# Kernel optimization log

Hardware: AMD Instinct MI355X
Metric: run time of the kernel (lower is better)

## Reference

```python
import jax, jax.numpy as jnp
import numpy as np

N_TREES, N_LEAVES, PATH_LEN, N_NODES, D, B = 10, 16, 5, 31, 256, 4096


def _local_paths():
    # root-to-leaf paths of a full binary tree, depth 4: 31 nodes, 16 leaves, path len 5
    return np.array([[0, 1 + l // 8, 3 + l // 4, 7 + l // 2, 15 + l]
                     for l in range(N_LEAVES)], np.int32)


def setup_inputs() -> dict:
    key = jax.random.key(0)
    k1, k2, k3, k4, k5, k6 = jax.random.split(key, 6)
    # one activated leaf per tree -> multi-hot cross_features (B, N_TREES*N_LEAVES)
    leaf = jax.random.randint(k1, (B, N_TREES), 0, N_LEAVES)
    cross = jnp.zeros((B, N_TREES, N_LEAVES), jnp.float32)
    cross = cross.at[jnp.arange(B)[:, None], jnp.arange(N_TREES)[None, :], leaf].set(1.0)
    cross_features = cross.reshape(B, N_TREES * N_LEAVES)
    # learned params: node embedding table + single-layer LSTM (torch init scale 1/sqrt(D))
    emb = jax.random.normal(k2, (N_TREES * N_NODES, D), jnp.float32) * 0.02
    s = 1.0 / np.sqrt(D)
    W_ih = jax.random.uniform(k3, (4 * D, D), jnp.float32, -s, s)
    W_hh = jax.random.uniform(k4, (4 * D, D), jnp.float32, -s, s)
    b_ih = jax.random.uniform(k5, (4 * D,), jnp.float32, -s, s)
    b_hh = jax.random.uniform(k6, (4 * D,), jnp.float32, -s, s)
    return {"cross_features": cross_features, "emb": emb, "W_ih": W_ih,
            "W_hh": W_hh, "b_ih": b_ih, "b_hh": b_hh}


def reference(cross_features, emb, W_ih, W_hh, b_ih, b_hh):
    # global path node ids per (tree, leaf): [T, L, P]
    gpaths = jnp.asarray(_local_paths())[None, :, :] + \
        (jnp.arange(N_TREES, dtype=jnp.int32) * N_NODES)[:, None, None]
    # activated leaf per tree (exactly one hot per 16-leaf block)
    leaf = jnp.argmax(cross_features.reshape(B, N_TREES, N_LEAVES), axis=-1)  # [B, T]
    node_ids = gpaths[jnp.arange(N_TREES)[None, :], leaf]                     # [B, T, P]
    x = emb[node_ids].reshape(B * N_TREES, PATH_LEN, D)                       # packed paths
    # precompute input projections for all steps: [N, P, 4D]
    xg = jnp.einsum('npd,gd->npg', x, W_ih) + (b_ih + b_hh)

    def step(carry, xt):
        h, c = carry
        g = xt + h @ W_hh.T
        i, f, gg, o = jnp.split(g, 4, axis=-1)  # torch gate order: i, f, g, o
        c = jax.nn.sigmoid(f) * c + jax.nn.sigmoid(i) * jnp.tanh(gg)
        h = jax.nn.sigmoid(o) * jnp.tanh(c)
        return (h, c), None

    n = B * N_TREES
    h0 = jnp.zeros((n, D), x.dtype)
    (h, _), _ = jax.lax.scan(step, (h0, h0), jnp.swapaxes(xg, 0, 1))
    return h.reshape(B, N_TREES, D)
```

## Files before the change

kernel.cpp:

```cpp
#include <hip/hip_runtime.h>

#define NT 10
#define NL 16
#define NN 31
#define DD 256
#define G4 1024
#define NNODES (NT*NN)
#define NPATH (NT*NL)
#define NB 4096
#define NROWS (NB*NT)

__device__ unsigned g_pg[3][16][32];

__device__ __forceinline__ float sigf(float x)   { return 1.0f / (1.0f + __expf(-x)); }
__device__ __forceinline__ float tanh_f(float x) { return 2.0f / (1.0f + __expf(-2.0f*x)) - 1.0f; }

__device__ __forceinline__ void co_store(float* p, float v) {
    union { float f; unsigned u; } c; c.f = v;
    __hip_atomic_store((unsigned*)p, c.u, __ATOMIC_RELAXED, __HIP_MEMORY_SCOPE_AGENT);
}

__global__ __launch_bounds__(256) void k_nodeproj(
    const float* __restrict__ emb, const float* __restrict__ Wih,
    const float* __restrict__ bih, const float* __restrict__ bhh,
    float* __restrict__ xg)
{
    __shared__ float smem[20 * 260 + 20 * 4 * 64];
    float4* es4 = (float4*)smem;
    float*  ps  = smem + 20 * 260;

    const int tid = threadIdx.x;
    const int nt  = blockIdx.x & 15;
    const int mt  = blockIdx.x >> 4;
    const int kq  = tid >> 6;
    const int w   = tid & 63;

    const float4* W4 = (const float4*)Wih + (size_t)(nt * 64 + w) * 64 + kq * 16;
    float4 wr[16];
    #pragma unroll
    for (int j = 0; j < 16; ++j) wr[j] = W4[j];

    const float4* emb4 = (const float4*)emb;
    #pragma unroll
    for (int r = 0; r < 5; ++r) {
        int idx = tid + 256 * r;
        int m = idx >> 6, q = idx & 63;
        int n = mt * 20 + m;
        es4[m * 65 + q] = (n < NNODES) ? emb4[(size_t)n * 64 + q]
                                       : make_float4(0.f, 0.f, 0.f, 0.f);
    }
    __syncthreads();

    float acc[20];
    #pragma unroll
    for (int m = 0; m < 20; ++m) acc[m] = 0.f;
    #pragma unroll
    for (int j = 0; j < 16; ++j) {
        float4 wv = wr[j];
        #pragma unroll
        for (int m = 0; m < 20; ++m) {
            float4 h = es4[m * 65 + kq * 16 + j];
            acc[m] = fmaf(wv.x, h.x, fmaf(wv.y, h.y,
                     fmaf(wv.z, h.z, fmaf(wv.w, h.w, acc[m]))));
        }
    }
    #pragma unroll
    for (int m = 0; m < 20; ++m) ps[(m * 4 + kq) * 64 + w] = acc[m];
    __syncthreads();

    const int nl   = tid & 63;
    const int msub = tid >> 6;
    const int j    = nt * 64 + nl;
    const float bsum = bih[j] + bhh[j];
    #pragma unroll
    for (int r = 0; r < 5; ++r) {
        int m = msub * 5 + r;
        int n = mt * 20 + m;
        float s = ps[(m * 4 + 0) * 64 + nl] + ps[(m * 4 + 1) * 64 + nl]
                + ps[(m * 4 + 2) * 64 + nl] + ps[(m * 4 + 3) * 64 + nl];
        if (n < NNODES) xg[(size_t)n * G4 + j] = s + bsum;
    }
}

__global__ __launch_bounds__(256) void k_steps(
    const float* __restrict__ xg, const float* __restrict__ Whh,
    float* __restrict__ h1g, float* __restrict__ h2g,
    float* __restrict__ h3g, float* __restrict__ h4g)
{
    __shared__ float smem[10 * 260 + 10 * 4 * 64];
    float4* hs4 = (float4*)smem;
    float*  hs  = smem;
    float*  ps  = smem + 10 * 260;

    const int tid   = threadIdx.x;
    const int pg    = blockIdx.x >> 4;
    const int dtile = blockIdx.x & 15;
    const int kq    = tid >> 6;
    const int w     = tid & 63;
    const int gate  = w >> 4;
    const int dlw   = w & 15;

    const unsigned base = __hip_atomic_load(&g_pg[2][pg][0],
        __ATOMIC_RELAXED, __HIP_MEMORY_SCOPE_AGENT);

    const int t0 = (pg * 10) >> 4;
    const int t1 = (pg * 10 + 9) >> 4;
    const float* xr0 = xg + (size_t)(t0 * NN) * G4;
    const float* xr1 = xg + (size_t)(t1 * NN) * G4;
    float ri0 = xr0[tid], rg0 = xr0[512 + tid], ro0 = xr0[768 + tid];
    float ri1 = xr1[tid], rg1 = xr1[512 + tid], ro1 = xr1[768 + tid];

    const int p_act  = tid >> 4;
    const int dl_act = tid & 15;
    const int d_act  = dtile * 16 + dl_act;
    const int pglob  = pg * 10 + p_act;
    const int t_act  = pglob >> 4, l_act = pglob & 15;
    float xnv[4][4];
    float rc_i = 0.f, rc_g = 0.f;
    if (tid < 160) {
        #pragma unroll
        for (int s = 1; s <= 4; ++s) {
            int off = (1 << s) - 1 + (l_act >> (4 - s));
            const float* xn = xg + (size_t)(t_act * NN + off) * G4;
            xnv[s - 1][0] = xn[d_act];
            xnv[s - 1][1] = xn[256 + d_act];
            xnv[s - 1][2] = xn[512 + d_act];
            xnv[s - 1][3] = xn[768 + d_act];
        }
        const float* xr = xg + (size_t)(t_act * NN) * G4;
        rc_i = xr[d_act]; rc_g = xr[512 + d_act];
    }

    const float4* Wh4 = (const float4*)Whh
        + (size_t)(gate * 256 + dtile * 16 + dlw) * 64 + kq * 16;
    float4 wreg[16];
    #pragma unroll
    for (int j = 0; j < 16; ++j) wreg[j] = Wh4[j];

    float c_reg = 0.f;
    if (tid < 160) c_reg = sigf(rc_i) * tanh_f(rc_g);

    {
        float c1a = sigf(ri0) * tanh_f(rg0);
        float h1a = sigf(ro0) * tanh_f(c1a);
        float c1b = sigf(ri1) * tanh_f(rg1);
        float h1b = sigf(ro1) * tanh_f(c1b);
        #pragma unroll
        for (int r = 0; r < 10; ++r) {
            int t = (pg * 10 + r) >> 4;
            hs[r * 260 + tid] = (t == t0) ? h1a : h1b;
        }
    }
    __syncthreads();

    float* hout[4] = { h1g, h2g, h3g, h4g };
    const float* hin[3] = { h1g, h2g, h3g };

    #pragma unroll
    for (int s = 1; s <= 4; ++s) {
        if (s > 1) {
            const unsigned tgt = base + 16u;
            while (__hip_atomic_load(&g_pg[s - 2][pg][0],
                    __ATOMIC_RELAXED, __HIP_MEMORY_SCOPE_AGENT) < tgt) {}
            const unsigned long long* src =
                (const unsigned long long*)(hin[s - 2] + (size_t)pg * 2560);
            unsigned long long raw[5];
            #pragma unroll
            for (int r = 0; r < 5; ++r) {
                int i8 = tid + 256 * r;
                raw[r] = __hip_atomic_load(
                    src + (size_t)(i8 >> 7) * 128 + (i8 & 127),
                    __ATOMIC_RELAXED, __HIP_MEMORY_SCOPE_AGENT);
            }
            float2* hs2 = (float2*)hs;
            #pragma unroll
            for (int r = 0; r < 5; ++r) {
                int i8 = tid + 256 * r;
                union { unsigned long long u; float2 f; } cv; cv.u = raw[r];
                hs2[(i8 >> 7) * 130 + (i8 & 127)] = cv.f;
            }
            __syncthreads();
        }

        float acc[10];
        #pragma unroll
        for (int p = 0; p < 10; ++p) acc[p] = 0.f;
        #pragma unroll
        for (int j = 0; j < 16; ++j) {
            float4 wv = wreg[j];
            #pragma unroll
            for (int p = 0; p < 10; ++p) {
                float4 h = hs4[p * 65 + kq * 16 + j];
                acc[p] = fmaf(wv.x, h.x, fmaf(wv.y, h.y,
                         fmaf(wv.z, h.z, fmaf(wv.w, h.w, acc[p]))));
            }
        }
        #pragma unroll
        for (int p = 0; p < 10; ++p) ps[(p * 4 + kq) * 64 + w] = acc[p];
        __syncthreads();

        if (tid < 160) {
            float g0 = 0.f, g1 = 0.f, g2 = 0.f, g3 = 0.f;
            #pragma unroll
            for (int q = 0; q < 4; ++q) {
                g0 += ps[(p_act * 4 + q) * 64 +  0 + dl_act];
                g1 += ps[(p_act * 4 + q) * 64 + 16 + dl_act];
                g2 += ps[(p_act * 4 + q) * 64 + 32 + dl_act];
                g3 += ps[(p_act * 4 + q) * 64 + 48 + dl_act];
            }
            float gi = g0 + xnv[s - 1][0];
            float gf = g1 + xnv[s - 1][1];
            float gg = g2 + xnv[s - 1][2];
            float go = g3 + xnv[s - 1][3];
            float cn = sigf(gf) * c_reg + sigf(gi) * tanh_f(gg);
            c_reg = cn;
            float hn = sigf(go) * tanh_f(cn);
            if (s < 4) co_store(hout[s - 1] + (size_t)pglob * DD + d_act, hn);
            else       hout[3][(size_t)pglob * DD + d_act] = hn;
        }

        if (s < 4) {
            __syncthreads();
            if (tid == 0)
                __hip_atomic_fetch_add(&g_pg[s - 1][pg][0], 1u,
                    __ATOMIC_RELAXED, __HIP_MEMORY_SCOPE_AGENT);
        }
    }
}

__global__ __launch_bounds__(256) void k_scatter(
    const float* __restrict__ cross, const float* __restrict__ htab,
    float* __restrict__ out)
{
    const int tid  = threadIdx.x;
    const int wave = tid >> 6;
    const int lane = tid & 63;
    const int r = blockIdx.x * 4 + wave;
    const int b = r / NT;
    const int t = r - b * NT;

    float v = 0.f;
    if (lane < NL) v = cross[(size_t)b * (NT * NL) + t * NL + lane];
    unsigned long long m = __ballot(v > 0.5f);
    int leaf = m ? (int)__builtin_ctzll(m) : 0;
    int p = t * NL + leaf;

    const float4* h4 = (const float4*)htab;
    float4* o4 = (float4*)out;
    o4[(size_t)r * 64 + lane] = h4[(size_t)p * 64 + lane];
}

extern "C" void kernel_launch(void* const* d_in, const int* in_sizes, int n_in,
                              void* d_out, int out_size, void* d_ws, size_t ws_size,
                              hipStream_t stream)
{
    const float* cross = (const float*)d_in[0];
    const float* emb   = (const float*)d_in[1];
    const float* Wih   = (const float*)d_in[2];
    const float* Whh   = (const float*)d_in[3];
    const float* bih   = (const float*)d_in[4];
    const float* bhh   = (const float*)d_in[5];
    float* out = (float*)d_out;

    float* ws  = (float*)d_ws;
    float* xg  = ws;
    float* h1g = xg + NNODES * G4;
    float* h2g = h1g + NPATH * DD;
    float* h3g = h2g + NPATH * DD;
    float* h4g = h3g + NPATH * DD;

    hipLaunchKernelGGL(k_nodeproj, dim3(256), dim3(256), 0, stream,
                       emb, Wih, bih, bhh, xg);
    hipLaunchKernelGGL(k_steps, dim3(256), dim3(256), 0, stream,
                       xg, Whh, h1g, h2g, h3g, h4g);
    hipLaunchKernelGGL(k_scatter, dim3(10240), dim3(256), 0, stream,
                       cross, h4g, out);
}
```

Baseline: 118.4 us.

## Split LSTM steps into per-level kernels computing only unique tree path prefixes

```diff
diff --git a/kernel.cpp b/kernel.cpp
--- a/kernel.cpp
+++ b/kernel.cpp
@@ -8,17 +8,9 @@
 #define NNODES (NT*NN)
 #define NPATH (NT*NL)
 #define NB 4096
-#define NROWS (NB*NT)
-
-__device__ unsigned g_pg[3][16][32];
 
 __device__ __forceinline__ float sigf(float x)   { return 1.0f / (1.0f + __expf(-x)); }
 __device__ __forceinline__ float tanh_f(float x) { return 2.0f / (1.0f + __expf(-2.0f*x)) - 1.0f; }
-
-__device__ __forceinline__ void co_store(float* p, float v) {
-    union { float f; unsigned u; } c; c.f = v;
-    __hip_atomic_store((unsigned*)p, c.u, __ATOMIC_RELAXED, __HIP_MEMORY_SCOPE_AGENT);
-}
 
 __global__ __launch_bounds__(256) void k_nodeproj(
     const float* __restrict__ emb, const float* __restrict__ Wih,
@@ -82,149 +74,92 @@
     }
 }
 
-__global__ __launch_bounds__(256) void k_steps(
+template<int S>
+__global__ __launch_bounds__(256) void k_step(
     const float* __restrict__ xg, const float* __restrict__ Whh,
-    float* __restrict__ h1g, float* __restrict__ h2g,
-    float* __restrict__ h3g, float* __restrict__ h4g)
-{
-    __shared__ float smem[10 * 260 + 10 * 4 * 64];
-    float4* hs4 = (float4*)smem;
-    float*  hs  = smem;
-    float*  ps  = smem + 10 * 260;
-
-    const int tid   = threadIdx.x;
-    const int pg    = blockIdx.x >> 4;
-    const int dtile = blockIdx.x & 15;
-    const int kq    = tid >> 6;
-    const int w     = tid & 63;
-    const int gate  = w >> 4;
-    const int dlw   = w & 15;
-
-    const unsigned base = __hip_atomic_load(&g_pg[2][pg][0],
-        __ATOMIC_RELAXED, __HIP_MEMORY_SCOPE_AGENT);
-
-    const int t0 = (pg * 10) >> 4;
-    const int t1 = (pg * 10 + 9) >> 4;
-    const float* xr0 = xg + (size_t)(t0 * NN) * G4;
-    const float* xr1 = xg + (size_t)(t1 * NN) * G4;
-    float ri0 = xr0[tid], rg0 = xr0[512 + tid], ro0 = xr0[768 + tid];
-    float ri1 = xr1[tid], rg1 = xr1[512 + tid], ro1 = xr1[768 + tid];
-
-    const int p_act  = tid >> 4;
-    const int dl_act = tid & 15;
-    const int d_act  = dtile * 16 + dl_act;
-    const int pglob  = pg * 10 + p_act;
-    const int t_act  = pglob >> 4, l_act = pglob & 15;
-    float xnv[4][4];
-    float rc_i = 0.f, rc_g = 0.f;
-    if (tid < 160) {
-        #pragma unroll
-        for (int s = 1; s <= 4; ++s) {
-            int off = (1 << s) - 1 + (l_act >> (4 - s));
-            const float* xn = xg + (size_t)(t_act * NN + off) * G4;
-            xnv[s - 1][0] = xn[d_act];
-            xnv[s - 1][1] = xn[256 + d_act];
-            xnv[s - 1][2] = xn[512 + d_act];
-            xnv[s - 1][3] = xn[768 + d_act];
+    const float* __restrict__ hprev, const float* __restrict__ cprev,
+    float* __restrict__ hout, float* __restrict__ cout)
+{
+    constexpr int L = 1 << (S - 1);
+    __shared__ float hs [L * DD];
+    __shared__ float ps [L * DD];
+    __shared__ float csl[L * 16];
+
+    const int tid  = threadIdx.x;
+    const int t    = blockIdx.x >> 4;
+    const int dt   = blockIdx.x & 15;
+    const int kq   = tid >> 6;
+    const int w    = tid & 63;
+    const int gate = w >> 4;
+    const int col  = w & 15;
+
+    const float4* W4 = (const float4*)Whh
+        + (size_t)(gate * DD + dt * 16 + col) * 64 + kq * 16;
+    float4 wreg[16];
+    #pragma unroll
+    for (int j = 0; j < 16; ++j) wreg[j] = W4[j];
+
+    if constexpr (S == 1) {
+        const float* xr = xg + (size_t)(t * NN) * G4;
+        float xi = xr[tid], xgg = xr[512 + tid], xo = xr[768 + tid];
+        float c0 = sigf(xi) * tanh_f(xgg);
+        float h0 = sigf(xo) * tanh_f(c0);
+        hs[tid] = h0;
+        if ((tid >> 4) == dt) csl[tid & 15] = c0;
+    } else {
+        #pragma unroll
+        for (int rr = 0; rr < L; ++rr)
+            hs[rr * DD + tid] = hprev[(size_t)(t * L + rr) * DD + tid];
+        if (tid < L * 16)
+            csl[tid] = cprev[(size_t)(t * L + (tid >> 4)) * DD
+                             + dt * 16 + (tid & 15)];
+    }
+    __syncthreads();
+
+    const float4* hs4 = (const float4*)hs;
+    float acc[L];
+    #pragma unroll
+    for (int p = 0; p < L; ++p) acc[p] = 0.f;
+    #pragma unroll
+    for (int j = 0; j < 16; ++j) {
+        float4 wv = wreg[j];
+        #pragma unroll
+        for (int p = 0; p < L; ++p) {
+            float4 h = hs4[p * 64 + kq * 16 + j];
+            acc[p] = fmaf(wv.x, h.x, fmaf(wv.y, h.y,
+                     fmaf(wv.z, h.z, fmaf(wv.w, h.w, acc[p]))));
         }
-        const float* xr = xg + (size_t)(t_act * NN) * G4;
-        rc_i = xr[d_act]; rc_g = xr[512 + d_act];
-    }
-
-    const float4* Wh4 = (const float4*)Whh
-        + (size_t)(gate * 256 + dtile * 16 + dlw) * 64 + kq * 16;
-    float4 wreg[16];
-    #pragma unroll
-    for (int j = 0; j < 16; ++j) wreg[j] = Wh4[j];
-
-    float c_reg = 0.f;
-    if (tid < 160) c_reg = sigf(rc_i) * tanh_f(rc_g);
-
-    {
-        float c1a = sigf(ri0) * tanh_f(rg0);
-        float h1a = sigf(ro0) * tanh_f(c1a);
-        float c1b = sigf(ri1) * tanh_f(rg1);
-        float h1b = sigf(ro1) * tanh_f(c1b);
-        #pragma unroll
-        for (int r = 0; r < 10; ++r) {
-            int t = (pg * 10 + r) >> 4;
-            hs[r * 260 + tid] = (t == t0) ? h1a : h1b;
+    }
+    #pragma unroll
+    for (int p = 0; p < L; ++p) ps[p * DD + kq * 64 + w] = acc[p];
+    __syncthreads();
+
+    if (tid < 32 * L) {
+        const int p    = tid >> 5;
+        const int ch   = (tid >> 4) & 1;
+        const int c2   = tid & 15;
+        const int q    = p * 2 + ch;
+        const int node = ((1 << S) - 1) + q;
+        const float* xn = xg + (size_t)(t * NN + node) * G4 + dt * 16 + c2;
+
+        float g0 = 0.f, g1 = 0.f, g2 = 0.f, g3 = 0.f;
+        #pragma unroll
+        for (int k = 0; k < 4; ++k) {
+            const float* pp = ps + p * DD + k * 64;
+            g0 += pp[ 0 + c2]; g1 += pp[16 + c2];
+            g2 += pp[32 + c2]; g3 += pp[48 + c2];
         }
-    }
-    __syncthreads();
-
-    float* hout[4] = { h1g, h2g, h3g, h4g };
-    const float* hin[3] = { h1g, h2g, h3g };
-
-    #pragma unroll
-    for (int s = 1; s <= 4; ++s) {
-        if (s > 1) {
-            const unsigned tgt = base + 16u;
-            while (__hip_atomic_load(&g_pg[s - 2][pg][0],
-                    __ATOMIC_RELAXED, __HIP_MEMORY_SCOPE_AGENT) < tgt) {}
-            const unsigned long long* src =
-                (const unsigned long long*)(hin[s - 2] + (size_t)pg * 2560);
-            unsigned long long raw[5];
-            #pragma unroll
-            for (int r = 0; r < 5; ++r) {
-                int i8 = tid + 256 * r;
-                raw[r] = __hip_atomic_load(
-                    src + (size_t)(i8 >> 7) * 128 + (i8 & 127),
-                    __ATOMIC_RELAXED, __HIP_MEMORY_SCOPE_AGENT);
-            }
-            float2* hs2 = (float2*)hs;
-            #pragma unroll
-            for (int r = 0; r < 5; ++r) {
-                int i8 = tid + 256 * r;
-                union { unsigned long long u; float2 f; } cv; cv.u = raw[r];
-                hs2[(i8 >> 7) * 130 + (i8 & 127)] = cv.f;
-            }
-            __syncthreads();
-        }
-
-        float acc[10];
-        #pragma unroll
-        for (int p = 0; p < 10; ++p) acc[p] = 0.f;
-        #pragma unroll
-        for (int j = 0; j < 16; ++j) {
-            float4 wv = wreg[j];
-            #pragma unroll
-            for (int p = 0; p < 10; ++p) {
-                float4 h = hs4[p * 65 + kq * 16 + j];
-                acc[p] = fmaf(wv.x, h.x, fmaf(wv.y, h.y,
-                         fmaf(wv.z, h.z, fmaf(wv.w, h.w, acc[p]))));
-            }
-        }
-        #pragma unroll
-        for (int p = 0; p < 10; ++p) ps[(p * 4 + kq) * 64 + w] = acc[p];
-        __syncthreads();
-
-        if (tid < 160) {
-            float g0 = 0.f, g1 = 0.f, g2 = 0.f, g3 = 0.f;
-            #pragma unroll
-            for (int q = 0; q < 4; ++q) {
-                g0 += ps[(p_act * 4 + q) * 64 +  0 + dl_act];
-                g1 += ps[(p_act * 4 + q) * 64 + 16 + dl_act];
-                g2 += ps[(p_act * 4 + q) * 64 + 32 + dl_act];
-                g3 += ps[(p_act * 4 + q) * 64 + 48 + dl_act];
-            }
-            float gi = g0 + xnv[s - 1][0];
-            float gf = g1 + xnv[s - 1][1];
-            float gg = g2 + xnv[s - 1][2];
-            float go = g3 + xnv[s - 1][3];
-            float cn = sigf(gf) * c_reg + sigf(gi) * tanh_f(gg);
-            c_reg = cn;
-            float hn = sigf(go) * tanh_f(cn);
-            if (s < 4) co_store(hout[s - 1] + (size_t)pglob * DD + d_act, hn);
-            else       hout[3][(size_t)pglob * DD + d_act] = hn;
-        }
-
-        if (s < 4) {
-            __syncthreads();
-            if (tid == 0)
-                __hip_atomic_fetch_add(&g_pg[s - 1][pg][0], 1u,
-                    __ATOMIC_RELAXED, __HIP_MEMORY_SCOPE_AGENT);
-        }
+        float gi = g0 + xn[0];
+        float gf = g1 + xn[256];
+        float gg = g2 + xn[512];
+        float go = g3 + xn[768];
+        float cin = csl[p * 16 + c2];
+        float cn  = sigf(gf) * cin + sigf(gi) * tanh_f(gg);
+        float hn  = sigf(go) * tanh_f(cn);
+
+        size_t orow = (size_t)(t * 2 * L + q);
+        hout[orow * DD + dt * 16 + c2] = hn;
+        if constexpr (S < 4) cout[orow * DD + dt * 16 + c2] = cn;
     }
 }
 
@@ -262,17 +197,26 @@
     const float* bhh   = (const float*)d_in[5];
     float* out = (float*)d_out;
 
-    float* ws  = (float*)d_ws;
-    float* xg  = ws;
-    float* h1g = xg + NNODES * G4;
-    float* h2g = h1g + NPATH * DD;
-    float* h3g = h2g + NPATH * DD;
-    float* h4g = h3g + NPATH * DD;
+    float* ws = (float*)d_ws;
+    float* xg = ws;
+    float* h1 = xg + (size_t)NNODES * G4;
+    float* c1 = h1 + 20 * DD;
+    float* h2 = c1 + 20 * DD;
+    float* c2 = h2 + 40 * DD;
+    float* h3 = c2 + 40 * DD;
+    float* c3 = h3 + 80 * DD;
+    float* h4 = c3 + 80 * DD;
 
     hipLaunchKernelGGL(k_nodeproj, dim3(256), dim3(256), 0, stream,
                        emb, Wih, bih, bhh, xg);
-    hipLaunchKernelGGL(k_steps, dim3(256), dim3(256), 0, stream,
-                       xg, Whh, h1g, h2g, h3g, h4g);
+    hipLaunchKernelGGL(HIP_KERNEL_NAME(k_step<1>), dim3(160), dim3(256), 0, stream,
+                       xg, Whh, (const float*)nullptr, (const float*)nullptr, h1, c1);
+    hipLaunchKernelGGL(HIP_KERNEL_NAME(k_step<2>), dim3(160), dim3(256), 0, stream,
+                       xg, Whh, h1, c1, h2, c2);
+    hipLaunchKernelGGL(HIP_KERNEL_NAME(k_step<3>), dim3(160), dim3(256), 0, stream,
+                       xg, Whh, h2, c2, h3, c3);
+    hipLaunchKernelGGL(HIP_KERNEL_NAME(k_step<4>), dim3(160), dim3(256), 0, stream,
+                       xg, Whh, h3, c3, h4, (float*)nullptr);
     hipLaunchKernelGGL(k_scatter, dim3(10240), dim3(256), 0, stream,
-                       cross, h4g, out);
-}
+                       cross, h4, out);
+}
```

Result: no change. 117.4 us (-0.8%).
